# Kernel tuning notes

Measured on AMD Instinct MI355X. Metric: run time of the kernel, lower is better.

Reference implementation:

```python
import jax, jax.numpy as jnp
import numpy as np

B, N, F, U, S = 64, 4096, 2, 16, 2


def setup_inputs() -> dict:
    key = jax.random.key(0)
    ks = jax.random.split(key, 7)
    inputs = jax.random.normal(ks[0], (B, F * N), dtype=jnp.float32)
    state = jax.random.normal(ks[1], (B, U * N), dtype=jnp.float32)

    def random_walk(k):
        a = jax.random.uniform(k, (N, N), dtype=jnp.float32)
        return a / jnp.sum(a, axis=1, keepdims=True)  # row-stochastic like D^-1 A

    support0 = random_walk(ks[2])
    support1 = random_walk(ks[3])
    kshape = ((F + U) * S, U)
    scale = jnp.float32(1.0 / np.sqrt(kshape[0]))
    r_kernel = jax.random.normal(ks[4], kshape, dtype=jnp.float32) * scale
    u_kernel = jax.random.normal(ks[5], kshape, dtype=jnp.float32) * scale
    c_kernel = jax.random.normal(ks[6], kshape, dtype=jnp.float32) * scale
    return {"inputs": inputs, "state": state, "support0": support0,
            "support1": support1, "r_kernel": r_kernel, "u_kernel": u_kernel,
            "c_kernel": c_kernel}


def _diffuse(x, supports):
    # x: (B, C, N); K.dot(x, support.T)[b,c,m] = sum_n x[b,c,n] * support[m,n]
    return jnp.concatenate([jnp.einsum('bcn,mn->bcm', x, s) for s in supports], axis=1)


def reference(inputs, state, support0, support1, r_kernel, u_kernel, c_kernel):
    supports = (support0, support1)
    feats = inputs.reshape(B, F, N)
    prev = state.reshape(B, U, N)

    h = _diffuse(feats, supports).transpose(0, 2, 1)   # (B, N, S*F)
    st = _diffuse(prev, supports).transpose(0, 2, 1)   # (B, N, S*U)
    hs = jnp.concatenate([h, st], axis=-1)             # (B, N, S*(F+U))

    r = jax.nn.sigmoid(hs @ r_kernel)                  # (B, N, U)
    u = jax.nn.sigmoid(hs @ u_kernel)                  # (B, N, U)

    prev_t = prev.transpose(0, 2, 1)                   # (B, N, U)
    r_prev = (r * prev_t).transpose(0, 2, 1)           # (B, U, N)
    c_state = _diffuse(r_prev, supports).transpose(0, 2, 1)  # (B, N, S*U)
    c = jnp.tanh(jnp.concatenate([h, c_state], axis=-1) @ c_kernel)  # (B, N, U)

    z = u * prev_t + (1.0 - u) * c                     # (B, N, U)
    # original: activation=None -> linear, then K.reshape(output, (-1, units*num_nodes))
    return z.reshape(B, U * N)
```

## Files before the change

kernel.cpp:

```cpp
#include <hip/hip_runtime.h>
#include <cstdint>

#define KDIM 4096
#define NNODE 4096
#define TSTEPS 128

typedef __bf16 bf16x8 __attribute__((ext_vector_type(8)));
typedef float floatx4 __attribute__((ext_vector_type(4)));

__device__ __forceinline__ uint16_t f2b(float f) {
  union { float f; uint32_t u; } v; v.f = f;
  uint32_t u = v.u;
  return (uint16_t)((u + 0x7FFFu + ((u >> 16) & 1u)) >> 16);
}
__device__ __forceinline__ float b2f(uint16_t h) {
  union { uint32_t u; float f; } v; v.u = ((uint32_t)h) << 16; return v.f;
}
__device__ __forceinline__ uint32_t pack2(float a, float b) {
  return (uint32_t)f2b(a) | ((uint32_t)f2b(b) << 16);
}


__global__ __launch_bounds__(256) void cvt_supports(
    const float* __restrict__ s0, const float* __restrict__ s1,
    uint16_t* __restrict__ d0, uint16_t* __restrict__ d1) {
  const float* src = blockIdx.z ? s1 : s0;
  uint16_t* dst = blockIdx.z ? d1 : d0;
  const int c16 = blockIdx.x, kb = blockIdx.y;
  const int col_in = threadIdx.x >> 4, k8 = threadIdx.x & 15;
  const int col = c16 * 16 + col_in;
  const int k = kb * 128 + k8 * 8;
  const float* p = src + (size_t)col * KDIM + k;
  float4 v0 = *(const float4*)p;
  float4 v1 = *(const float4*)(p + 4);
  uint4 o;
  o.x = pack2(v0.x, v0.y); o.y = pack2(v0.z, v0.w);
  o.z = pack2(v1.x, v1.y); o.w = pack2(v1.z, v1.w);
  size_t off = ((size_t)(c16 * 128 + kb * 4 + (k8 >> 2))) * 512 +
               (size_t)((k8 & 3) * 16 + col_in) * 8;
  *(uint4*)(dst + off) = o;
}

__global__ __launch_bounds__(256) void pack_x1(
    const float* __restrict__ inp, const float* __restrict__ st,
    uint16_t* __restrict__ X1) {
  const int r16 = blockIdx.x, kb = blockIdx.y;
  const int row_in = threadIdx.x >> 4, k8 = threadIdx.x & 15;
  const int row = r16 * 16 + row_in;
  const int k = kb * 128 + k8 * 8;
  int b = row / 18, c = row - b * 18;
  const float* p = (c < 2) ? (inp + (size_t)b * 8192 + (size_t)c * 4096 + k)
                           : (st + (size_t)b * 65536 + (size_t)(c - 2) * 4096 + k);
  float4 v0 = *(const float4*)p;
  float4 v1 = *(const float4*)(p + 4);
  uint4 o;
  o.x = pack2(v0.x, v0.y); o.y = pack2(v0.z, v0.w);
  o.z = pack2(v1.x, v1.y); o.w = pack2(v1.z, v1.w);
  size_t off = ((size_t)(r16 * 128 + kb * 4 + (k8 >> 2))) * 512 +
               (size_t)((k8 & 3) * 16 + row_in) * 8;
  *(uint4*)(X1 + off) = o;
}

__device__ __forceinline__ void gl_lds16(const uint16_t* g, uint16_t* l) {
  __builtin_amdgcn_global_load_lds(
      (const __attribute__((address_space(1))) uint32_t*)g,
      (__attribute__((address_space(3))) uint32_t*)l, 16, 0, 0);
}

template <int MODE>
__global__ __launch_bounds__(512, 2) void gemm_frag(
    const uint16_t* __restrict__ Af, const uint16_t* __restrict__ S0f,
    const uint16_t* __restrict__ S1f, uint16_t* __restrict__ D) {
  constexpr int CPB   = (MODE == 1) ? 18 : 16;
  constexpr int OUTC  = (MODE == 1) ? 36 : 32;
  constexpr int MFR   = (MODE == 1) ? 9 : 8;
  constexpr int WM    = (MODE == 1) ? 1 : 2;
  constexpr int WN    = 8 / WM;
  constexpr int AR    = MFR / WM;
  constexpr int BR    = 16 / WN;
  constexpr int NREAL = MFR + 16;
  constexpr int SLOTS = (NREAL + 7) & ~7;
  constexpr int LPW   = SLOTS / 8;
  constexpr int NCH   = TSTEPS;

  __shared__ uint16_t sAB[4][SLOTS][512];

  const int lane = threadIdx.x & 63, wave = threadIdx.x >> 6;
  const int wr = wave / WN, wc = wave % WN;
  const int s = blockIdx.z;
  const uint16_t* __restrict__ Bf = s ? S1f : S0f;
  const int yF = blockIdx.y * MFR;
  const int xF = blockIdx.x * 16;

  const uint16_t* Gp[LPW];
#pragma unroll
  for (int i = 0; i < LPW; ++i) {
    int sid = wave * LPW + i;
    const uint16_t* base;
    int fr;
    if (sid < MFR)        { base = Af; fr = yF + sid; }
    else if (sid < NREAL) { base = Bf; fr = xF + sid - MFR; }
    else                  { base = Af; fr = yF; }
    Gp[i] = base + (size_t)fr * (TSTEPS * 512) + (size_t)lane * 8;
  }

  floatx4 acc[AR][BR];
#pragma unroll
  for (int i = 0; i < AR; ++i)
#pragma unroll
    for (int j = 0; j < BR; ++j) acc[i][j] = (floatx4){0.f, 0.f, 0.f, 0.f};

  auto STAGE = [&](int bi, int c) {
    uint16_t* l = &sAB[bi][wave * LPW][0];
    const size_t off = (size_t)c * 512;
#pragma unroll
    for (int i = 0; i < LPW; ++i)
      gl_lds16(Gp[i] + off, l + (size_t)i * 512);
  };

  auto LDREG = [&](int bi, bf16x8* a, bf16x8* b) {
    const uint16_t* base = &sAB[bi][0][lane * 8];
#pragma unroll
    for (int rt = 0; rt < AR; ++rt)
      a[rt] = *(const bf16x8*)(base + (size_t)(wr * AR + rt) * 512);
#pragma unroll
    for (int ct = 0; ct < BR; ++ct)
      b[ct] = *(const bf16x8*)(base + (size_t)(MFR + wc * BR + ct) * 512);
  };

  auto MFMAALL = [&](bf16x8* a, bf16x8* b) {
    __builtin_amdgcn_s_setprio(1);
#pragma unroll
    for (int rt = 0; rt < AR; ++rt)
#pragma unroll
      for (int ct = 0; ct < BR; ++ct)
        acc[rt][ct] = __builtin_amdgcn_mfma_f32_16x16x32_bf16(
            a[rt], b[ct], acc[rt][ct], 0, 0, 0);
    __builtin_amdgcn_s_setprio(0);
  };

  auto waitVM = [&] {
    if constexpr (MODE == 1) asm volatile("s_waitcnt vmcnt(8)" ::: "memory");
    else                     asm volatile("s_waitcnt vmcnt(6)" ::: "memory");
  };
  auto waitLG = [&] {
    if constexpr (MODE == 1) asm volatile("s_waitcnt lgkmcnt(11)" ::: "memory");
    else                     asm volatile("s_waitcnt lgkmcnt(8)" ::: "memory");
  };

  STAGE(0, 0);
  STAGE(1, 1);
  STAGE(2, 2);
  waitVM();
  __builtin_amdgcn_sched_barrier(0);
  __builtin_amdgcn_s_barrier();
  __builtin_amdgcn_sched_barrier(0);
  bf16x8 aA[AR], bA[BR], aB[AR], bB[BR];
  LDREG(0, aA, bA);

#define GITER(J, SB, RB, CA, CB, NA, NB)                                    \
  {                                                                         \
    int cl = c0 + 3 + (J);                                                  \
    if (cl > NCH - 1) cl = NCH - 1;       \
    STAGE((SB), cl);                                                        \
    waitVM();                                                               \
    __builtin_amdgcn_sched_barrier(0);                                      \
    __builtin_amdgcn_s_barrier();                                           \
    __builtin_amdgcn_sched_barrier(0);                                      \
    LDREG((RB), NA, NB);                                                    \
    waitLG();                                                               \
    __builtin_amdgcn_sched_barrier(0);                                      \
    MFMAALL(CA, CB);                                                        \
    __builtin_amdgcn_sched_barrier(0);                                      \
  }

  for (int m = 0; m < NCH / 4; ++m) {
    const int c0 = m * 4;
    GITER(0, 3, 1, aA, bA, aB, bB)
    GITER(1, 0, 2, aB, bB, aA, bA)
    GITER(2, 1, 3, aA, bA, aB, bB)
    GITER(3, 2, 0, aB, bB, aA, bA)
  }
#undef GITER

#pragma unroll
  for (int rt = 0; rt < AR; ++rt) {
#pragma unroll
    for (int r = 0; r < 4; ++r) {
      int rowg = (yF + wr * AR + rt) * 16 + (lane >> 4) * 4 + r;
      int b = rowg / CPB, c = rowg - b * CPB;
      int jj;
      if (MODE == 1) jj = (c < 2) ? (2 * s + c) : (4 + 16 * s + (c - 2));
      else jj = 16 * s + c;
      uint16_t* drow = D + (size_t)(b * OUTC + jj) * NNODE;
#pragma unroll
      for (int ct = 0; ct < BR; ++ct) {
        int colg = xF * 16 + (wc * BR + ct) * 16 + (lane & 15);
        drow[colg] = f2b(acc[rt][ct][r]);
      }
    }
  }
}

__global__ __launch_bounds__(256) void stage2(
    const uint16_t* __restrict__ P1, const float* __restrict__ state,
    const float* __restrict__ rk, const float* __restrict__ uk,
    uint16_t* __restrict__ X2f, float* __restrict__ U) {
  __shared__ float s_rk[576], s_uk[576];
  __shared__ uint16_t s_x2[16 * 264];
  for (int i = threadIdx.x; i < 576; i += 256) { s_rk[i] = rk[i]; s_uk[i] = uk[i]; }
  __syncthreads();
  const int b = blockIdx.x >> 4, nb = blockIdx.x & 15;
  const int i = threadIdx.x;
  const int n = nb * 256 + i;
  float hs[36];
  const uint16_t* p = P1 + (size_t)b * 36 * NNODE + n;
#pragma unroll
  for (int j = 0; j < 36; ++j)
    hs[j] = b2f(p[(size_t)j * NNODE]);
  float ar[16], au[16];
#pragma unroll
  for (int k = 0; k < 16; ++k) { ar[k] = 0.f; au[k] = 0.f; }
#pragma unroll
  for (int j = 0; j < 36; ++j) {
    float h = hs[j];
#pragma unroll
    for (int k = 0; k < 16; ++k) {
      ar[k] += h * s_rk[j * 16 + k];
      au[k] += h * s_uk[j * 16 + k];
    }
  }
  const float* sp = state + (size_t)b * 65536 + n;
#pragma unroll
  for (int k = 0; k < 16; ++k) {
    float r = 1.f / (1.f + __expf(-ar[k]));
    float uu = 1.f / (1.f + __expf(-au[k]));
    float prev = sp[(size_t)k * NNODE];
    s_x2[k * 264 + i] = f2b(r * prev);
    U[(size_t)(b * 16 + k) * NNODE + n] = uu;
  }
  __syncthreads();
  uint16_t* region = X2f + ((size_t)b * 128 + nb * 8) * 512;
#pragma unroll
  for (int rr = 0; rr < 2; ++rr) {
    int fid = rr * 256 + i;
    int kk = fid & 15, qq = (fid >> 4) & 3, tl = fid >> 6;
    uint4 v = *(const uint4*)&s_x2[kk * 264 + tl * 32 + qq * 8];
    *(uint4*)(region + (size_t)fid * 8) = v;
  }
}

__global__ __launch_bounds__(256) void stage4(
    const uint16_t* __restrict__ P1, const uint16_t* __restrict__ P3,
    const float* __restrict__ U, const float* __restrict__ state,
    const float* __restrict__ ck, float* __restrict__ out) {
  __shared__ float s_ck[576];
  for (int i = threadIdx.x; i < 576; i += 256) s_ck[i] = ck[i];
  __syncthreads();
  int idx = blockIdx.x * 256 + threadIdx.x;
  int b = idx >> 12, n = idx & 4095;
  float hv[36];
  const uint16_t* p1 = P1 + (size_t)b * 36 * NNODE + n;
#pragma unroll
  for (int j = 0; j < 4; ++j)
    hv[j] = b2f(p1[(size_t)j * NNODE]);
  const uint16_t* p3 = P3 + (size_t)b * 32 * NNODE + n;
#pragma unroll
  for (int j = 0; j < 32; ++j)
    hv[4 + j] = b2f(p3[(size_t)j * NNODE]);
  float ac[16];
#pragma unroll
  for (int k = 0; k < 16; ++k) ac[k] = 0.f;
#pragma unroll
  for (int j = 0; j < 36; ++j) {
    float h = hv[j];
#pragma unroll
    for (int k = 0; k < 16; ++k) ac[k] += h * s_ck[j * 16 + k];
  }
  const float* sp = state + (size_t)b * 65536 + n;
  const float* up = U + (size_t)b * 16 * NNODE + n;
  float z[16];
#pragma unroll
  for (int k = 0; k < 16; ++k) {
    float e = __expf(2.f * ac[k]);
    float c = 1.f - 2.f / (e + 1.f);
    float uu = up[(size_t)k * NNODE];
    float prev = sp[(size_t)k * NNODE];
    z[k] = uu * prev + (1.f - uu) * c;
  }
  float4* po = (float4*)(out + (size_t)b * 65536 + (size_t)n * 16);
#pragma unroll
  for (int k4 = 0; k4 < 4; ++k4)
    po[k4] = make_float4(z[k4 * 4], z[k4 * 4 + 1], z[k4 * 4 + 2], z[k4 * 4 + 3]);
}

extern "C" void kernel_launch(void* const* d_in, const int* in_sizes, int n_in,
                              void* d_out, int out_size, void* d_ws, size_t ws_size,
                              hipStream_t stream) {
  const float* inputs = (const float*)d_in[0];
  const float* state = (const float*)d_in[1];
  const float* s0 = (const float*)d_in[2];
  const float* s1 = (const float*)d_in[3];
  const float* rk = (const float*)d_in[4];
  const float* uk = (const float*)d_in[5];
  const float* ck = (const float*)d_in[6];
  float* out = (float*)d_out;
  char* ws = (char*)d_ws;

  uint16_t* S0f = (uint16_t*)(ws);
  uint16_t* S1f = (uint16_t*)(ws + 33554432);
  uint16_t* X1f = (uint16_t*)(ws + 67108864);
  uint16_t* X2f = (uint16_t*)(ws + 67108864);
  uint16_t* P1 = (uint16_t*)(ws + 76546048);
  float* U = (float*)(ws + 114294784);
  uint16_t* P3 = (uint16_t*)(ws + 131072000);

  cvt_supports<<<dim3(256, 32, 2), 256, 0, stream>>>(s0, s1, S0f, S1f);
  pack_x1<<<dim3(72, 32), 256, 0, stream>>>(inputs, state, X1f);
  gemm_frag<1><<<dim3(16, 8, 2), 512, 0, stream>>>(X1f, S0f, S1f, P1);
  stage2<<<1024, 256, 0, stream>>>(P1, state, rk, uk, X2f, U);
  gemm_frag<3><<<dim3(16, 8, 2), 512, 0, stream>>>(X2f, S0f, S1f, P3);
  stage4<<<1024, 256, 0, stream>>>(P1, P3, U, state, ck, out);
}
```

Before: 345.6 us.

## Split GEMM K dimension in two and enlarge M tile, sum partials downstream

The two diffusion GEMMs now split the 128-step K loop into two halves across blockIdx.z, writing separate bf16 partial outputs that stage2 and stage4 add together on load. Each block covers twice as many A fragments (18/16 rows), with a fixed 2x4 wave layout and a single A register set loaded per iteration while B is double-buffered. The aim is more A/B reuse per block and a reshaped LDS pipeline at the same grid size. In exchange it doubles the partial-output traffic, needs extra loads in the epilogue kernels, and adds bf16 rounding of each partial. It also enlarges the LDS footprint per block and assumes the workspace has room for the second partial buffer.

```diff
diff --git a/kernel.cpp b/kernel.cpp
--- a/kernel.cpp
+++ b/kernel.cpp
@@ -73,35 +73,36 @@
     const uint16_t* __restrict__ S1f, uint16_t* __restrict__ D) {
   constexpr int CPB   = (MODE == 1) ? 18 : 16;
   constexpr int OUTC  = (MODE == 1) ? 36 : 32;
-  constexpr int MFR   = (MODE == 1) ? 9 : 8;
-  constexpr int WM    = (MODE == 1) ? 1 : 2;
-  constexpr int WN    = 8 / WM;
-  constexpr int AR    = MFR / WM;
-  constexpr int BR    = 16 / WN;
+  constexpr int MFR   = (MODE == 1) ? 18 : 16;
+  constexpr int AR    = MFR / 2;
+  constexpr int BR    = 4;
   constexpr int NREAL = MFR + 16;
-  constexpr int SLOTS = (NREAL + 7) & ~7;
-  constexpr int LPW   = SLOTS / 8;
-  constexpr int NCH   = TSTEPS;
-
-  __shared__ uint16_t sAB[4][SLOTS][512];
+  constexpr int EXTRA = NREAL - 32;
+  constexpr int NCH   = 64;
+  constexpr size_t PSTRIDE = (size_t)64 * OUTC * NNODE;
+
+  __shared__ uint16_t sAB[4][NREAL][512];
 
   const int lane = threadIdx.x & 63, wave = threadIdx.x >> 6;
-  const int wr = wave / WN, wc = wave % WN;
-  const int s = blockIdx.z;
+  const int wr = wave >> 2, wc = wave & 3;
+  const int s = blockIdx.z & 1, ks = blockIdx.z >> 1;
   const uint16_t* __restrict__ Bf = s ? S1f : S0f;
   const int yF = blockIdx.y * MFR;
   const int xF = blockIdx.x * 16;
-
-  const uint16_t* Gp[LPW];
-#pragma unroll
-  for (int i = 0; i < LPW; ++i) {
-    int sid = wave * LPW + i;
-    const uint16_t* base;
-    int fr;
-    if (sid < MFR)        { base = Af; fr = yF + sid; }
-    else if (sid < NREAL) { base = Bf; fr = xF + sid - MFR; }
-    else                  { base = Af; fr = yF; }
-    Gp[i] = base + (size_t)fr * (TSTEPS * 512) + (size_t)lane * 8;
+  const int tBeg = ks * NCH;
+
+  const int lpw = (EXTRA && wave < EXTRA) ? 5 : 4;
+  const int slotbase = 4 * wave + (wave < EXTRA ? wave : EXTRA);
+
+  const uint16_t* Gp[5];
+#pragma unroll
+  for (int i = 0; i < 5; ++i) {
+    int sid = slotbase + i;
+    if (i < lpw && sid < NREAL) {
+      const uint16_t* base = (sid < MFR) ? Af : Bf;
+      int fr = (sid < MFR) ? (yF + sid) : (xF + (sid - MFR));
+      Gp[i] = base + ((size_t)fr * TSTEPS + tBeg) * 512 + (size_t)lane * 8;
+    } else Gp[i] = Af;
   }
 
   floatx4 acc[AR][BR];
@@ -111,18 +112,21 @@
     for (int j = 0; j < BR; ++j) acc[i][j] = (floatx4){0.f, 0.f, 0.f, 0.f};
 
   auto STAGE = [&](int bi, int c) {
-    uint16_t* l = &sAB[bi][wave * LPW][0];
+    uint16_t* l = &sAB[bi][slotbase][0];
     const size_t off = (size_t)c * 512;
 #pragma unroll
-    for (int i = 0; i < LPW; ++i)
-      gl_lds16(Gp[i] + off, l + (size_t)i * 512);
-  };
-
-  auto LDREG = [&](int bi, bf16x8* a, bf16x8* b) {
+    for (int i = 0; i < 5; ++i)
+      if (i < lpw) gl_lds16(Gp[i] + off, l + (size_t)i * 512);
+  };
+
+  auto LDREG_A = [&](int bi, bf16x8* a) {
     const uint16_t* base = &sAB[bi][0][lane * 8];
 #pragma unroll
     for (int rt = 0; rt < AR; ++rt)
       a[rt] = *(const bf16x8*)(base + (size_t)(wr * AR + rt) * 512);
+  };
+  auto LDREG_B = [&](int bi, bf16x8* b) {
+    const uint16_t* base = &sAB[bi][0][lane * 8];
 #pragma unroll
     for (int ct = 0; ct < BR; ++ct)
       b[ct] = *(const bf16x8*)(base + (size_t)(MFR + wc * BR + ct) * 512);
@@ -140,12 +144,12 @@
   };
 
   auto waitVM = [&] {
-    if constexpr (MODE == 1) asm volatile("s_waitcnt vmcnt(8)" ::: "memory");
-    else                     asm volatile("s_waitcnt vmcnt(6)" ::: "memory");
-  };
-  auto waitLG = [&] {
-    if constexpr (MODE == 1) asm volatile("s_waitcnt lgkmcnt(11)" ::: "memory");
-    else                     asm volatile("s_waitcnt lgkmcnt(8)" ::: "memory");
+    if constexpr (EXTRA > 0) {
+      if (wave < EXTRA) asm volatile("s_waitcnt vmcnt(10)" ::: "memory");
+      else              asm volatile("s_waitcnt vmcnt(8)" ::: "memory");
+    } else {
+      asm volatile("s_waitcnt vmcnt(8)" ::: "memory");
+    }
   };
 
   STAGE(0, 0);
@@ -155,34 +159,36 @@
   __builtin_amdgcn_sched_barrier(0);
   __builtin_amdgcn_s_barrier();
   __builtin_amdgcn_sched_barrier(0);
-  bf16x8 aA[AR], bA[BR], aB[AR], bB[BR];
-  LDREG(0, aA, bA);
-
-#define GITER(J, SB, RB, CA, CB, NA, NB)                                    \
+  bf16x8 aR[AR], bA[BR], bB[BR];
+  LDREG_B(0, bA);
+
+#define GITER(J, STB, ABUF, BBUF, CURB, NXTB)                               \
   {                                                                         \
     int cl = c0 + 3 + (J);                                                  \
     if (cl > NCH - 1) cl = NCH - 1;       \
-    STAGE((SB), cl);                                                        \
+    STAGE((STB), cl);                                                       \
     waitVM();                                                               \
     __builtin_amdgcn_sched_barrier(0);                                      \
     __builtin_amdgcn_s_barrier();                                           \
     __builtin_amdgcn_sched_barrier(0);                                      \
-    LDREG((RB), NA, NB);                                                    \
-    waitLG();                                                               \
+    LDREG_A((ABUF), aR);                                                    \
+    LDREG_B((BBUF), NXTB);                                                  \
+    asm volatile("s_waitcnt lgkmcnt(4)" ::: "memory");                      \
     __builtin_amdgcn_sched_barrier(0);                                      \
-    MFMAALL(CA, CB);                                                        \
+    MFMAALL(aR, CURB);                                                      \
     __builtin_amdgcn_sched_barrier(0);                                      \
   }
 
   for (int m = 0; m < NCH / 4; ++m) {
     const int c0 = m * 4;
-    GITER(0, 3, 1, aA, bA, aB, bB)
-    GITER(1, 0, 2, aB, bB, aA, bA)
-    GITER(2, 1, 3, aA, bA, aB, bB)
-    GITER(3, 2, 0, aB, bB, aA, bA)
+    GITER(0, 3, 0, 1, bA, bB)
+    GITER(1, 0, 1, 2, bB, bA)
+    GITER(2, 1, 2, 3, bA, bB)
+    GITER(3, 2, 3, 0, bB, bA)
   }
 #undef GITER
 
+  uint16_t* Dp = D + (size_t)ks * PSTRIDE;
 #pragma unroll
   for (int rt = 0; rt < AR; ++rt) {
 #pragma unroll
@@ -192,10 +198,10 @@
       int jj;
       if (MODE == 1) jj = (c < 2) ? (2 * s + c) : (4 + 16 * s + (c - 2));
       else jj = 16 * s + c;
-      uint16_t* drow = D + (size_t)(b * OUTC + jj) * NNODE;
+      uint16_t* drow = Dp + (size_t)(b * OUTC + jj) * NNODE;
 #pragma unroll
       for (int ct = 0; ct < BR; ++ct) {
-        int colg = xF * 16 + (wc * BR + ct) * 16 + (lane & 15);
+        int colg = (xF + wc * BR + ct) * 16 + (lane & 15);
         drow[colg] = f2b(acc[rt][ct][r]);
       }
     }
@@ -206,6 +212,7 @@
     const uint16_t* __restrict__ P1, const float* __restrict__ state,
     const float* __restrict__ rk, const float* __restrict__ uk,
     uint16_t* __restrict__ X2f, float* __restrict__ U) {
+  constexpr size_t PS = (size_t)64 * 36 * NNODE;
   __shared__ float s_rk[576], s_uk[576];
   __shared__ uint16_t s_x2[16 * 264];
   for (int i = threadIdx.x; i < 576; i += 256) { s_rk[i] = rk[i]; s_uk[i] = uk[i]; }
@@ -217,7 +224,7 @@
   const uint16_t* p = P1 + (size_t)b * 36 * NNODE + n;
 #pragma unroll
   for (int j = 0; j < 36; ++j)
-    hs[j] = b2f(p[(size_t)j * NNODE]);
+    hs[j] = b2f(p[(size_t)j * NNODE]) + b2f(p[PS + (size_t)j * NNODE]);
   float ar[16], au[16];
 #pragma unroll
   for (int k = 0; k < 16; ++k) { ar[k] = 0.f; au[k] = 0.f; }
@@ -254,6 +261,8 @@
     const uint16_t* __restrict__ P1, const uint16_t* __restrict__ P3,
     const float* __restrict__ U, const float* __restrict__ state,
     const float* __restrict__ ck, float* __restrict__ out) {
+  constexpr size_t PS1 = (size_t)64 * 36 * NNODE;
+  constexpr size_t PS3 = (size_t)64 * 32 * NNODE;
   __shared__ float s_ck[576];
   for (int i = threadIdx.x; i < 576; i += 256) s_ck[i] = ck[i];
   __syncthreads();
@@ -263,11 +272,11 @@
   const uint16_t* p1 = P1 + (size_t)b * 36 * NNODE + n;
 #pragma unroll
   for (int j = 0; j < 4; ++j)
-    hv[j] = b2f(p1[(size_t)j * NNODE]);
+    hv[j] = b2f(p1[(size_t)j * NNODE]) + b2f(p1[PS1 + (size_t)j * NNODE]);
   const uint16_t* p3 = P3 + (size_t)b * 32 * NNODE + n;
 #pragma unroll
   for (int j = 0; j < 32; ++j)
-    hv[4 + j] = b2f(p3[(size_t)j * NNODE]);
+    hv[4 + j] = b2f(p3[(size_t)j * NNODE]) + b2f(p3[PS3 + (size_t)j * NNODE]);
   float ac[16];
 #pragma unroll
   for (int k = 0; k < 16; ++k) ac[k] = 0.f;
@@ -317,8 +326,8 @@
 
   cvt_supports<<<dim3(256, 32, 2), 256, 0, stream>>>(s0, s1, S0f, S1f);
   pack_x1<<<dim3(72, 32), 256, 0, stream>>>(inputs, state, X1f);
-  gemm_frag<1><<<dim3(16, 8, 2), 512, 0, stream>>>(X1f, S0f, S1f, P1);
+  gemm_frag<1><<<dim3(16, 4, 4), 512, 0, stream>>>(X1f, S0f, S1f, P1);
   stage2<<<1024, 256, 0, stream>>>(P1, state, rk, uk, X2f, U);
-  gemm_frag<3><<<dim3(16, 8, 2), 512, 0, stream>>>(X2f, S0f, S1f, P3);
+  gemm_frag<3><<<dim3(16, 4, 4), 512, 0, stream>>>(X2f, S0f, S1f, P3);
   stage4<<<1024, 256, 0, stream>>>(P1, P3, U, state, ck, out);
 }
```

Result: slower. 439.3 us (+27.1%).
